# Kernel optimization log

Measured on AMD Instinct MI355X. Metric: run time of the kernel, lower is better.

The kernel has to match this reference:

```python
import jax, jax.numpy as jnp
import numpy as np

B, T_ENC, T_DEC = 16, 256, 64
N_MEL = 80
ENC_DIM = 512
ATTN_RNN_DIM = 1024
DEC_RNN_DIM = 1024
PRENET_DIM = 256
ATTN_DIM = 128
LOC_FILTERS = 32
LOC_KERNEL = 31


def setup_inputs() -> dict:
    key = jax.random.key(0)
    ks = jax.random.split(key, 32)
    s = 0.02
    inp = {
        "memory": jax.random.normal(ks[0], (B, T_ENC, ENC_DIM), jnp.float32),
        "decoder_inputs": jax.random.normal(ks[1], (B, N_MEL, T_DEC), jnp.float32),
        "memory_lengths": jax.random.randint(ks[2], (B,), T_ENC // 2, T_ENC + 1, jnp.int32),
        # prenet
        "prenet_W1": jax.random.normal(ks[3], (PRENET_DIM, N_MEL), jnp.float32) * s,
        "prenet_b1": jnp.zeros((PRENET_DIM,), jnp.float32),
        "prenet_W2": jax.random.normal(ks[4], (PRENET_DIM, PRENET_DIM), jnp.float32) * s,
        "prenet_b2": jnp.zeros((PRENET_DIM,), jnp.float32),
        # attention LSTMCell: input = prenet_dim + enc_dim
        "attn_rnn_Wih": jax.random.normal(ks[5], (4 * ATTN_RNN_DIM, PRENET_DIM + ENC_DIM), jnp.float32) * s,
        "attn_rnn_Whh": jax.random.normal(ks[6], (4 * ATTN_RNN_DIM, ATTN_RNN_DIM), jnp.float32) * s,
        "attn_rnn_bih": jnp.zeros((4 * ATTN_RNN_DIM,), jnp.float32),
        "attn_rnn_bhh": jnp.zeros((4 * ATTN_RNN_DIM,), jnp.float32),
        # attention projections (bias-free, Tacotron2 style)
        "query_W": jax.random.normal(ks[7], (ATTN_DIM, ATTN_RNN_DIM), jnp.float32) * s,
        "mem_W": jax.random.normal(ks[8], (ATTN_DIM, ENC_DIM), jnp.float32) * s,
        "loc_conv_W": jax.random.normal(ks[9], (LOC_FILTERS, 2, LOC_KERNEL), jnp.float32) * s,
        "loc_dense_W": jax.random.normal(ks[10], (ATTN_DIM, LOC_FILTERS), jnp.float32) * s,
        "attn_v": jax.random.normal(ks[11], (1, ATTN_DIM), jnp.float32) * s,
        # decoder LSTMCell: input = attn_rnn_dim + enc_dim
        "dec_rnn_Wih": jax.random.normal(ks[12], (4 * DEC_RNN_DIM, ATTN_RNN_DIM + ENC_DIM), jnp.float32) * s,
        "dec_rnn_Whh": jax.random.normal(ks[13], (4 * DEC_RNN_DIM, DEC_RNN_DIM), jnp.float32) * s,
        "dec_rnn_bih": jnp.zeros((4 * DEC_RNN_DIM,), jnp.float32),
        "dec_rnn_bhh": jnp.zeros((4 * DEC_RNN_DIM,), jnp.float32),
        # output heads
        "proj_W": jax.random.normal(ks[14], (N_MEL, DEC_RNN_DIM + ENC_DIM), jnp.float32) * s,
        "proj_b": jnp.zeros((N_MEL,), jnp.float32),
        "gate_W": jax.random.normal(ks[15], (1, DEC_RNN_DIM + ENC_DIM), jnp.float32) * s,
        "gate_b": jnp.zeros((1,), jnp.float32),
    }
    return inp


def _lstm_cell(x, h, c, Wih, Whh, bih, bhh):
    gates = x @ Wih.T + bih + h @ Whh.T + bhh  # [B, 4H]
    i, f, g, o = jnp.split(gates, 4, axis=-1)
    c2 = jax.nn.sigmoid(f) * c + jax.nn.sigmoid(i) * jnp.tanh(g)
    h2 = jax.nn.sigmoid(o) * jnp.tanh(c2)
    return h2, c2


def _decoder_forward(memory, decoder_inputs, memory_lengths,
                     prenet_W1, prenet_b1, prenet_W2, prenet_b2,
                     attn_rnn_Wih, attn_rnn_Whh, attn_rnn_bih, attn_rnn_bhh,
                     query_W, mem_W, loc_conv_W, loc_dense_W, attn_v,
                     dec_rnn_Wih, dec_rnn_Whh, dec_rnn_bih, dec_rnn_bhh,
                     proj_W, proj_b, gate_W, gate_b):
    b, t_enc, _ = memory.shape
    t_dec = decoder_inputs.shape[2]
    # parse_decoder_inputs: [B,80,T] -> [T,B,80]; prepend go frame
    frames = jnp.transpose(decoder_inputs, (2, 0, 1))  # [T,B,80]
    go = jnp.zeros((1, b, N_MEL), frames.dtype)
    frames = jnp.concatenate([go, frames], axis=0)  # [T+1,B,80]
    # prenet (dropout disabled for determinism)
    pre = jax.nn.relu(frames @ prenet_W1.T + prenet_b1)
    pre = jax.nn.relu(pre @ prenet_W2.T + prenet_b2)  # [T+1,B,256]
    pre = pre[:-1]  # steps use frames 0..T-1

    processed_memory = memory @ mem_W.T  # [B,T_enc,128]
    pad_mask = jnp.arange(t_enc)[None, :] >= memory_lengths[:, None]  # [B,T_enc] True=pad

    pad = (LOC_KERNEL - 1) // 2

    def step(carry, x_t):
        (ah, ac, dh, dc, aw, aw_cum, ctx) = carry
        cell_in = jnp.concatenate([x_t, ctx], axis=-1)
        ah, ac = _lstm_cell(cell_in, ah, ac, attn_rnn_Wih, attn_rnn_Whh, attn_rnn_bih, attn_rnn_bhh)
        # location-sensitive attention
        awc = jnp.stack([aw, aw_cum], axis=1)  # [B,2,T_enc]
        loc = jax.lax.conv_general_dilated(
            awc, loc_conv_W, window_strides=(1,), padding=[(pad, pad)],
            dimension_numbers=("NCH", "OIH", "NCH"))  # [B,32,T_enc]
        loc = jnp.transpose(loc, (0, 2, 1)) @ loc_dense_W.T  # [B,T_enc,128]
        query = (ah @ query_W.T)[:, None, :]  # [B,1,128]
        energies = jnp.squeeze(jnp.tanh(query + processed_memory + loc) @ attn_v.T, -1)  # [B,T_enc]
        energies = jnp.where(pad_mask, -1e9, energies)
        aw = jax.nn.softmax(energies, axis=1)
        ctx = jnp.einsum("bt,btd->bd", aw, memory)
        aw_cum = aw_cum + aw
        dec_in = jnp.concatenate([ah, ctx], axis=-1)
        dh, dc = _lstm_cell(dec_in, dh, dc, dec_rnn_Wih, dec_rnn_Whh, dec_rnn_bih, dec_rnn_bhh)
        dhc = jnp.concatenate([dh, ctx], axis=-1)
        mel = dhc @ proj_W.T + proj_b  # [B,80]
        gate = jnp.squeeze(dhc @ gate_W.T + gate_b, -1)  # [B]
        return (ah, ac, dh, dc, aw, aw_cum, ctx), (mel, gate, aw)

    z = jnp.zeros
    carry0 = (z((b, ATTN_RNN_DIM)), z((b, ATTN_RNN_DIM)),
              z((b, DEC_RNN_DIM)), z((b, DEC_RNN_DIM)),
              z((b, t_enc)), z((b, t_enc)), z((b, ENC_DIM)))
    _, (mels, gates, aligns) = jax.lax.scan(step, carry0, pre)
    # parse_decoder_outputs
    mel_outputs = jnp.transpose(mels, (1, 2, 0))  # [B,80,T_dec]
    gate_outputs = jnp.transpose(gates, (1, 0))  # [B,T_dec]
    alignments = jnp.transpose(aligns, (1, 0, 2))  # [B,T_dec,T_enc]
    return mel_outputs, gate_outputs, alignments


def reference(memory, decoder_inputs, memory_lengths,
              prenet_W1, prenet_b1, prenet_W2, prenet_b2,
              attn_rnn_Wih, attn_rnn_Whh, attn_rnn_bih, attn_rnn_bhh,
              query_W, mem_W, loc_conv_W, loc_dense_W, attn_v,
              dec_rnn_Wih, dec_rnn_Whh, dec_rnn_bih, dec_rnn_bhh,
              proj_W, proj_b, gate_W, gate_b):
    return _decoder_forward(memory, decoder_inputs, memory_lengths,
                            prenet_W1, prenet_b1, prenet_W2, prenet_b2,
                            attn_rnn_Wih, attn_rnn_Whh, attn_rnn_bih, attn_rnn_bhh,
                            query_W, mem_W, loc_conv_W, loc_dense_W, attn_v,
                            dec_rnn_Wih, dec_rnn_Whh, dec_rnn_bih, dec_rnn_bhh,
                            proj_W, proj_b, gate_W, gate_b)
```

## Files before the change

### kernel.cpp

```cpp
#include <hip/hip_runtime.h>

typedef __attribute__((ext_vector_type(8))) short short8;
typedef __attribute__((ext_vector_type(4))) float f32x4;
typedef unsigned short u16;
typedef unsigned int u32;
typedef unsigned long long u64;


static constexpr size_t OFF_WFA   = 0;
static constexpr size_t OFF_WFD   = 14680064;
static constexpr size_t OFF_PREF  = 35651584;
static constexpr size_t OFF_QWB   = 36175872;
static constexpr size_t OFF_MWT   = 36438016;
static constexpr size_t OFF_BA    = 36700160;
static constexpr size_t OFF_BD    = 36716544;
static constexpr size_t OFF_PM    = 36732928;
static constexpr size_t OFF_CTXF  = 38830080;
static constexpr size_t OFF_DHF   = 40960000;
static constexpr size_t OFF_AHFD  = 45219840;
static constexpr size_t OFF_CTXFD = 47349760;
static constexpr size_t OFF_DHFD  = 48414720;
static constexpr size_t OFF_BAR   = 50544640;
static constexpr size_t OFF_END   = 50548736;

__device__ __forceinline__ float sigmf(float x) { return 1.f / (1.f + expf(-x)); }
__device__ __forceinline__ float tanh_fast(float x) {
  float e2 = __expf(2.f * x);
  return 1.f - 2.f / (e2 + 1.f);
}
__device__ __forceinline__ u16 f2bf(float f) {
  u32 u = __float_as_uint(f);
  return (u16)((u + 0x7FFFu + ((u >> 16) & 1u)) >> 16);
}
__device__ __forceinline__ float bf2f(u16 x) { return __uint_as_float(((u32)x) << 16); }

__device__ __forceinline__ short8 ld_frag_nt(const void* p) {
  const u64* q = (const u64*)p;
  u64 lo = __builtin_nontemporal_load(q);
  u64 hi = __builtin_nontemporal_load(q + 1);
  union { u64 q2[2]; short8 s; } u;
  u.q2[0] = lo; u.q2[1] = hi;
  return u.s;
}

__device__ __forceinline__ void st_u16_agent(u16* p, u16 v) {
  __hip_atomic_store(p, v, __ATOMIC_RELAXED, __HIP_MEMORY_SCOPE_AGENT);
}
__device__ __forceinline__ void st_f32_agent(float* p, float v) {
  __hip_atomic_store(p, v, __ATOMIC_RELAXED, __HIP_MEMORY_SCOPE_AGENT);
}
__device__ __forceinline__ u32 ld_u32_agent(const u32* p) {
  return __hip_atomic_load(p, __ATOMIC_RELAXED, __HIP_MEMORY_SCOPE_AGENT);
}
__device__ __forceinline__ void st_u32_agent(u32* p, u32 v) {
  __hip_atomic_store(p, v, __ATOMIC_RELAXED, __HIP_MEMORY_SCOPE_AGENT);
}

template <int SLP>
__device__ __forceinline__ void wait_p128(const u32* F, u32 target, int th) {
  if (th < 64) {
    for (;;) {
      u32 v0 = ld_u32_agent(F + th);
      u32 v1 = ld_u32_agent(F + 64 + th);
      u32 mn = v0 < v1 ? v0 : v1;
      if (__all(mn >= target)) break;
      __builtin_amdgcn_s_sleep(SLP);
    }
  }
  __syncthreads();
}
template <int SLP>
__device__ __forceinline__ void wait_s16(const u32* F, u32 target, int th) {
  if (th < 64) {
    const u32* pf = F + (th & 15) * 16;
    for (;;) {
      u32 v = ld_u32_agent(pf);
      if (__all(v >= target)) break;
      __builtin_amdgcn_s_sleep(SLP);
    }
  }
  __syncthreads();
}

__global__ void k_wfrag(const float* __restrict__ Wih, const float* __restrict__ Whh,
                        char* __restrict__ dst, int NT, int Kih) {
  int idx = blockIdx.x * 256 + threadIdx.x;
  int l = idx & 63;
  int st = idx >> 6;
  int s = st % NT, tile = st / NT;
  int r = l & 15, kg = l >> 4;
  int j = (r >> 2) * 1024 + tile * 4 + (r & 3);
  int k0 = s * 32 + kg * 8;
  const float* src = (k0 < Kih) ? (Wih + (size_t)j * Kih + k0)
                                : (Whh + (size_t)j * 1024 + (k0 - Kih));
  short8 v;
#pragma unroll
  for (int e = 0; e < 8; ++e) v[e] = (short)f2bf(src[e]);
  *(short8*)(dst + (size_t)idx * 16) = v;
}

__global__ void k_smallprep(const float* __restrict__ memW,
                            const float* __restrict__ abih, const float* __restrict__ abhh,
                            const float* __restrict__ dbih, const float* __restrict__ dbhh,
                            const float* __restrict__ qW, char* __restrict__ wsb) {
  int idx = blockIdx.x * 256 + threadIdx.x;
  if (idx < 65536) {
    int k = idx >> 7, d = idx & 127;
    ((float*)(wsb + OFF_MWT))[idx] = memW[d * 512 + k];
  } else if (idx < 69632) {
    int j = idx - 65536;
    ((float*)(wsb + OFF_BA))[j] = abih[j] + abhh[j];
  } else if (idx < 73728) {
    int j = idx - 69632;
    ((float*)(wsb + OFF_BD))[j] = dbih[j] + dbhh[j];
  } else if (idx < 204800) {
    int j = idx - 73728;
    ((u16*)(wsb + OFF_QWB))[j] = f2bf(qW[j]);
  }
}

__global__ void k_prenet(const float* __restrict__ dec_in,
                         const float* __restrict__ W1, const float* __restrict__ b1,
                         const float* __restrict__ W2, const float* __restrict__ b2,
                         char* __restrict__ wsb) {
  int s = blockIdx.x, b = blockIdx.y, th = threadIdx.x;
  __shared__ float frame[80];
  __shared__ float h1[256];
  if (th < 80) frame[th] = (s == 0) ? 0.f : dec_in[(b * 80 + th) * 64 + (s - 1)];
  __syncthreads();
  float a = b1[th];
  const float* w1r = W1 + th * 80;
  for (int m = 0; m < 80; ++m) a += w1r[m] * frame[m];
  h1[th] = fmaxf(a, 0.f);
  __syncthreads();
  float a2 = b2[th];
  const float* w2r = W2 + th * 256;
  for (int i = 0; i < 256; ++i) a2 += w2r[i] * h1[i];
  float pre = fmaxf(a2, 0.f);
  int k = th;
  ((u16*)(wsb + OFF_PREF))[(((size_t)s * 8 + (k >> 5)) * 64 + ((k >> 3) & 3) * 16 + b) * 8 + (k & 7)] = f2bf(pre);
}

__global__ void k_pm(const float* __restrict__ memory, char* __restrict__ wsb) {
  int bk = blockIdx.x, th = threadIdx.x;
  int b = bk >> 4, t0 = (bk & 15) * 16;
  __shared__ float mrow[16 * 512];
  for (int i = 0; i < 8; ++i) {
    int fi4 = i * 256 + th;
    int tl = fi4 >> 7, k4 = (fi4 & 127) << 2;
    *(float4*)&mrow[tl * 512 + k4] =
        *(const float4*)&memory[((size_t)(b * 256 + t0 + tl)) * 512 + k4];
  }
  __syncthreads();
  int d = th & 127, tl0 = th >> 7;
  float acc[8] = {};
  const float* mWT = (const float*)(wsb + OFF_MWT);
  float* pmw = (float*)(wsb + OFF_PM);
  for (int k = 0; k < 512; ++k) {
    float w = mWT[k * 128 + d];
#pragma unroll
    for (int i = 0; i < 8; ++i) acc[i] += w * mrow[(tl0 + i * 2) * 512 + k];
  }
  for (int i = 0; i < 8; ++i)
    pmw[((size_t)(b * 256 + t0 + tl0 + i * 2)) * 128 + d] = acc[i];
}

struct KParams {
  const float* memory;
  const int* mlen;
  const float* convW;
  const float* ldW;
  const float* attnv;
  const float* projW;
  const float* projb;
  const float* gateW;
  const float* gateb;
  char* wsb;
  float* out;
};

__device__ __forceinline__ f32x4 attn_early(char* wsb, int t, int kc, int l,
                                            const short8* afE) {
  f32x4 acc = {0.f, 0.f, 0.f, 0.f};
#pragma unroll
  for (int i = 0; i < 10; ++i) {
    int pe = kc * 10 + i;
    const char* src = (pe < 8)
        ? wsb + OFF_PREF + (((size_t)t * 8 + pe) * 64 + l) * 16
        : wsb + OFF_AHFD + (((size_t)t * 32 + (pe - 8)) * 64 + l) * 16;
    short8 bv = ld_frag_nt(src);
    acc = __builtin_amdgcn_mfma_f32_16x16x32_bf16(afE[i], bv, acc, 0, 0, 0);
  }
  return acc;
}

__device__ __forceinline__ void run_dec(char* wsb, int t, int tb, int th, int l, int w,
                                        int rt, int kc, float biasD_r, float& cD,
                                        float* smC) {
  const char* wfd = wsb + OFF_WFD;
  int tIdx = tb * 2 + rt;
  f32x4 acc = {0.f, 0.f, 0.f, 0.f};
#pragma unroll
  for (int i = 0; i < 20; ++i) {
    int kt = kc * 20 + i;
    short8 av = *(const short8*)(wfd + (((size_t)tIdx * 80 + kt) * 64 + l) * 16);
    const char* src;
    if (kt < 32)      src = wsb + OFF_AHFD + (((size_t)t * 32 + kt) * 64 + l) * 16;
    else if (kt < 48) src = wsb + OFF_CTXFD + (((size_t)t * 16 + (kt - 32)) * 64 + l) * 16;
    else              src = wsb + OFF_DHFD + (((size_t)(t - 1) * 32 + (kt - 48)) * 64 + l) * 16;
    short8 bv = ld_frag_nt(src);
    acc = __builtin_amdgcn_mfma_f32_16x16x32_bf16(av, bv, acc, 0, 0, 0);
  }
#pragma unroll
  for (int r4 = 0; r4 < 4; ++r4)
    smC[w * 256 + ((l >> 4) * 4 + r4) * 16 + (l & 15)] = acc[r4];
  __syncthreads();
  {
    int rt2 = th >> 8, r = (th >> 4) & 15, b2 = th & 15;
    float s = 0.f;
#pragma unroll
    for (int q = 0; q < 4; ++q) s += smC[(q * 2 + rt2) * 256 + r * 16 + b2];
    smC[4096 + th] = s + biasD_r;
  }
  __syncthreads();
  if (th < 128) {
    int b = th & 15, lu = th >> 4;
    int rt3 = lu >> 2, ul = lu & 3;
    int u = (tb * 2 + rt3) * 4 + ul;
    float gi = smC[4096 + rt3 * 256 + ul * 16 + b];
    float gf = smC[4096 + rt3 * 256 + (4 + ul) * 16 + b];
    float gc = smC[4096 + rt3 * 256 + (8 + ul) * 16 + b];
    float go = smC[4096 + rt3 * 256 + (12 + ul) * 16 + b];
    float c2 = sigmf(gf) * cD + sigmf(gi) * tanhf(gc);
    float h2 = sigmf(go) * tanhf(c2);
    cD = c2;
    st_f32_agent((float*)(wsb + OFF_DHF) + ((size_t)t * 1024 + u) * 16 + b, h2);
    st_u16_agent((u16*)(wsb + OFF_DHFD) +
                 ((((size_t)t * 32 + (u >> 5)) * 64 + ((u >> 3) & 3) * 16 + b) * 8 + (u & 7)),
                 f2bf(h2));
  }
}

__global__ void __launch_bounds__(512, 1) k_main(KParams p) {
  const int th = threadIdx.x;
  const int bk = blockIdx.x;
  char* wsb = p.wsb;
  const int l = th & 63, w = th >> 6;
  u32* Af = (u32*)(wsb + OFF_BAR);
  u32* Df = (u32*)(wsb + OFF_BAR + 1024);
  u32* Bf = (u32*)(wsb + OFF_BAR + 2048);

  __shared__ float smC[4608];
  __shared__ float s2q[128], s2v[128];
  __shared__ u16 s_convF[8192];
  __shared__ __align__(16) float s2ah[1024];
  __shared__ float s_e[256], s3wr[4];
  __shared__ float s1cw[1984];
  __shared__ float s_aw[256], s_awc[256];

  const float* pm = (const float*)(wsb + OFF_PM);
  const u16* qwb = (const u16*)(wsb + OFF_QWB);

  if (bk < 16) {
    for (int i = th; i < 1984; i += 512) s1cw[i] = p.convW[i];
    for (int i = th; i < 4096; i += 512) ((u32*)s_convF)[i] = 0u;
    if (th < 128) s2v[th] = p.attnv[th];
    if (th < 256) { s_aw[th] = 0.f; s_awc[th] = 0.f; }
  }

  float biasA_r = 0.f, biasD_r = 0.f;
  if (bk >= 16 && bk < 144) {
    int r = (th >> 4) & 15, rt2 = th >> 8, tbase = (bk - 16) * 2;
    biasA_r = ((const float*)(wsb + OFF_BA))[(r >> 2) * 1024 + (tbase + rt2) * 4 + (r & 3)];
    biasD_r = ((const float*)(wsb + OFF_BD))[(r >> 2) * 1024 + (tbase + rt2) * 4 + (r & 3)];
  }
  int lenB = 0;
  if (bk < 16) lenB = p.mlen[bk];
  float cA = 0.f, cD = 0.f;

  const int rt = w & 1, kc = w >> 1;
  short8 afE[10], afL[4];
  if (bk >= 16 && bk < 144) {
    const char* wfa = wsb + OFF_WFA;
    int tIdx = (bk - 16) * 2 + rt;
#pragma unroll
    for (int i = 0; i < 10; ++i) {
      int pe = kc * 10 + i;
      int kt = (pe < 8) ? pe : (24 + (pe - 8));
      afE[i] = *(const short8*)(wfa + (((size_t)tIdx * 56 + kt) * 64 + l) * 16);
    }
#pragma unroll
    for (int i = 0; i < 4; ++i) {
      int kt = 8 + kc * 4 + i;
      afL[i] = *(const short8*)(wfa + (((size_t)tIdx * 56 + kt) * 64 + l) * 16);
    }
  }
  short8 ldwB[8];
  if (bk < 16) {
    int kg = l >> 4, dcol = l & 15;
#pragma unroll
    for (int dt = 0; dt < 8; ++dt) {
      short8 v;
#pragma unroll
      for (int e = 0; e < 8; ++e)
        v[e] = (short)f2bf(p.ldW[(dt * 16 + dcol) * 32 + kg * 8 + e]);
      ldwB[dt] = v;
    }
  }
  __syncthreads();

  if (bk >= 16 && bk < 144) {
    const int tb = bk - 16;
    f32x4 acc = attn_early(wsb, 0, kc, l, afE);
    for (int t = 0; t < 64; ++t) {
      wait_s16<4>(Bf, (u32)t, th);
#pragma unroll
      for (int i = 0; i < 4; ++i) {
        int ct = kc * 4 + i;
        short8 bv = ld_frag_nt(wsb + OFF_CTXFD + (((size_t)t * 16 + ct) * 64 + l) * 16);
        acc = __builtin_amdgcn_mfma_f32_16x16x32_bf16(afL[i], bv, acc, 0, 0, 0);
      }
#pragma unroll
      for (int r4 = 0; r4 < 4; ++r4)
        smC[w * 256 + ((l >> 4) * 4 + r4) * 16 + (l & 15)] = acc[r4];
      __syncthreads();
      {
        int rt2 = th >> 8, r = (th >> 4) & 15, b2 = th & 15;
        float s = 0.f;
#pragma unroll
        for (int q = 0; q < 4; ++q) s += smC[(q * 2 + rt2) * 256 + r * 16 + b2];
        smC[4096 + th] = s + biasA_r;
      }
      __syncthreads();
      if (th < 128) {
        int b = th & 15, lu = th >> 4;
        int rt3 = lu >> 2, ul = lu & 3;
        int u = (tb * 2 + rt3) * 4 + ul;
        float gi = smC[4096 + rt3 * 256 + ul * 16 + b];
        float gf = smC[4096 + rt3 * 256 + (4 + ul) * 16 + b];
        float gc = smC[4096 + rt3 * 256 + (8 + ul) * 16 + b];
        float go = smC[4096 + rt3 * 256 + (12 + ul) * 16 + b];
        float c2 = sigmf(gf) * cA + sigmf(gi) * tanhf(gc);
        float h2 = sigmf(go) * tanhf(c2);
        cA = c2;
        st_u16_agent((u16*)(wsb + OFF_AHFD) +
                     ((((size_t)(t + 1) * 32 + (u >> 5)) * 64 + ((u >> 3) & 3) * 16 + b) * 8 + (u & 7)),
                     f2bf(h2));
      }
      __syncthreads();
      if (th == 0) st_u32_agent(Af + tb, (u32)(t + 1));
      if (t >= 1) {
        wait_p128<4>(Df, (u32)(t - 1), th);
        run_dec(wsb, t, tb, th, l, w, rt, kc, biasD_r, cD, smC);
        __syncthreads();
        if (th == 0) st_u32_agent(Df + tb, (u32)t);
      }
      if (t < 63) {
        wait_p128<4>(Af, (u32)(t + 1), th);
        acc = attn_early(wsb, t + 1, kc, l, afE);
      }
    }
    wait_s16<4>(Bf, 64u, th);
    wait_p128<4>(Df, 63u, th);
    run_dec(wsb, 64, tb, th, l, w, rt, kc, biasD_r, cD, smC);
    __syncthreads();
    if (th == 0) st_u32_agent(Df + tb, 64u);
  } else if (bk < 16) {
    const int b = bk;
    for (int t = 0; t < 64; ++t) {
      {
        int jmax = (lenB + 15) >> 4;
        for (int j = 0; j < jmax; ++j) {
          int idx = j * 512 + th, tt = idx >> 5, f = idx & 31;
          float a = 0.f;
          const float* w0 = s1cw + f * 62;
#pragma unroll
          for (int kk = 0; kk < 31; ++kk) {
            int pos = tt + kk - 15;
            bool ok = (pos >= 0 && pos < 256);
            float awv = ok ? s_aw[pos] : 0.f;
            float awcv = ok ? s_awc[pos] : 0.f;
            a += awv * w0[kk] + awcv * w0[31 + kk];
          }
          s_convF[(tt >> 4) * 512 + ((f >> 3) * 16 + (tt & 15)) * 8 + (f & 7)] = f2bf(a);
        }
      }
      wait_p128<4>(Af, (u32)(t + 1), th);
      if (th < 128) {
        int o = th;
        short8 v = ld_frag_nt(wsb + OFF_AHFD +
                    (((size_t)(t + 1) * 32 + (o >> 2)) * 64 + (o & 3) * 16 + b) * 16);
#pragma unroll
        for (int e = 0; e < 8; ++e) s2ah[o * 8 + e] = bf2f((u16)v[e]);
      }
      __syncthreads();
      {
        int d = th & 127, part = th >> 7;
        const u16* qr = qwb + d * 1024 + part * 256;
        const float* ah = s2ah + part * 256;
        float qa = 0.f;
        for (int kk = 0; kk < 256; kk += 8) {
          short8 v = *(const short8*)(qr + kk);
#pragma unroll
          for (int e = 0; e < 8; ++e) qa += bf2f((u16)v[e]) * ah[kk + e];
        }
        smC[part * 128 + d] = qa;
      }
      __syncthreads();
      if (th < 128) s2q[th] = smC[th] + smC[128 + th] + smC[256 + th] + smC[384 + th];
      __syncthreads();
      {
#pragma unroll
        for (int tl = 0; tl < 2; ++tl) {
          int ttile = w * 2 + tl;
          short8 afc = *(const short8*)&s_convF[ttile * 512 + l * 8];
          int dcol = l & 15;
          float e0 = 0.f, e1 = 0.f, e2 = 0.f, e3 = 0.f;
          const float* pmb = pm + ((size_t)(b * 256 + ttile * 16 + (l >> 4) * 4)) * 128 + dcol;
#pragma unroll
          for (int dt = 0; dt < 8; ++dt) {
            f32x4 S = {0.f, 0.f, 0.f, 0.f};
            S = __builtin_amdgcn_mfma_f32_16x16x32_bf16(afc, ldwB[dt], S, 0, 0, 0);
            int d = dt * 16 + dcol;
            float qd = s2q[d], vd = s2v[d];
            e0 += vd * tanh_fast(qd + pmb[dt * 16 + 0 * 128] + S[0]);
            e1 += vd * tanh_fast(qd + pmb[dt * 16 + 1 * 128] + S[1]);
            e2 += vd * tanh_fast(qd + pmb[dt * 16 + 2 * 128] + S[2]);
            e3 += vd * tanh_fast(qd + pmb[dt * 16 + 3 * 128] + S[3]);
          }
#pragma unroll
          for (int off = 8; off; off >>= 1) {
            e0 += __shfl_xor(e0, off);
            e1 += __shfl_xor(e1, off);
            e2 += __shfl_xor(e2, off);
            e3 += __shfl_xor(e3, off);
          }
          if ((l & 15) == 0) {
            int tb0 = ttile * 16 + (l >> 4) * 4;
            s_e[tb0]     = (tb0     < lenB) ? __expf(e0) : 0.f;
            s_e[tb0 + 1] = (tb0 + 1 < lenB) ? __expf(e1) : 0.f;
            s_e[tb0 + 2] = (tb0 + 2 < lenB) ? __expf(e2) : 0.f;
            s_e[tb0 + 3] = (tb0 + 3 < lenB) ? __expf(e3) : 0.f;
          }
        }
      }
      __syncthreads();
      if (th < 256) {
        float v0 = s_e[th];
#pragma unroll
        for (int off = 32; off; off >>= 1) v0 += __shfl_xor(v0, off);
        if ((th & 63) == 0) s3wr[th >> 6] = v0;
      }
      __syncthreads();
      float rden = 1.f / (s3wr[0] + s3wr[1] + s3wr[2] + s3wr[3]);
      if (th < 256) {
        float a = s_e[th] * rden;
        s_aw[th] = a;
        s_awc[th] += a;
        p.out[82944 + ((size_t)(b * 64 + t)) * 256 + th] = a;
      }
      __syncthreads();
      {
        int dq = th & 127, tg = th >> 7;
        int d0 = dq * 4;
        float a0 = 0.f, a1 = 0.f, a2 = 0.f, a3 = 0.f;
        const float* mb = p.memory + ((size_t)b * 256) * 512 + d0;
        for (int tt = tg; tt < lenB; tt += 4) {
          float4 mv = *(const float4*)(mb + (size_t)tt * 512);
          float aw = s_aw[tt];
          a0 += aw * mv.x; a1 += aw * mv.y; a2 += aw * mv.z; a3 += aw * mv.w;
        }
        smC[tg * 512 + d0]     = a0;
        smC[tg * 512 + d0 + 1] = a1;
        smC[tg * 512 + d0 + 2] = a2;
        smC[tg * 512 + d0 + 3] = a3;
      }
      __syncthreads();
      {
        int d = th;
        float ctxv = smC[d] + smC[512 + d] + smC[1024 + d] + smC[1536 + d];
        st_f32_agent((float*)(wsb + OFF_CTXF) + ((size_t)(t + 1) * 512 + d) * 16 + b, ctxv);
        st_u16_agent((u16*)(wsb + OFF_CTXFD) +
                     ((((size_t)(t + 1) * 16 + (d >> 5)) * 64 + ((d >> 3) & 3) * 16 + b) * 8 + (d & 7)),
                     f2bf(ctxv));
      }
      __syncthreads();
      if (th == 0) st_u32_agent(Bf + b * 16, (u32)(t + 1));
    }
  }

  if (bk >= 144) {
    wait_p128<96>(Df, 64u, th);
    wait_s16<96>(Bf, 64u, th);
  } else {
    wait_p128<8>(Df, 64u, th);
    wait_s16<8>(Bf, 64u, th);
  }
  {
    int t = bk & 63, pa = bk >> 6;
    const float* dh = (const float*)(wsb + OFF_DHF) + (size_t)(t + 1) * 16384;
    const float* cx = (const float*)(wsb + OFF_CTXF) + (size_t)(t + 1) * 8192;
    int lim = (pa == 3) ? 336 : 320;
    for (int idx = th; idx < lim; idx += 512) {
      if (idx < 320) {
        int mi = idx >> 4, b = idx & 15, m = pa * 20 + mi;
        const float* wr = p.projW + (size_t)m * 1536;
        float a0 = 0.f, a1 = 0.f;
#pragma unroll 8
        for (int k = 0; k < 1024; k += 2) { a0 += wr[k] * dh[k * 16 + b]; a1 += wr[k + 1] * dh[(k + 1) * 16 + b]; }
#pragma unroll 8
        for (int k = 0; k < 512; k += 2)  { a0 += wr[1024 + k] * cx[k * 16 + b]; a1 += wr[1025 + k] * cx[(k + 1) * 16 + b]; }
        p.out[((size_t)(b * 80 + m)) * 64 + t] = a0 + a1 + p.projb[m];
      } else {
        int b = idx - 320;
        float a0 = 0.f, a1 = 0.f;
#pragma unroll 8
        for (int k = 0; k < 1024; k += 2) { a0 += p.gateW[k] * dh[k * 16 + b]; a1 += p.gateW[k + 1] * dh[(k + 1) * 16 + b]; }
#pragma unroll 8
        for (int k = 0; k < 512; k += 2)  { a0 += p.gateW[1024 + k] * cx[k * 16 + b]; a1 += p.gateW[1025 + k] * cx[(k + 1) * 16 + b]; }
        p.out[81920 + b * 64 + t] = a0 + a1 + p.gateb[0];
      }
    }
  }
}

extern "C" void kernel_launch(void* const* d_in, const int* in_sizes, int n_in,
                              void* d_out, int out_size, void* d_ws, size_t ws_size,
                              hipStream_t stream) {
  (void)in_sizes; (void)n_in; (void)out_size; (void)ws_size;
  const float* memory = (const float*)d_in[0];
  const float* dec_in = (const float*)d_in[1];
  const int*   mlen   = (const int*)d_in[2];
  const float* pW1    = (const float*)d_in[3];
  const float* pb1    = (const float*)d_in[4];
  const float* pW2    = (const float*)d_in[5];
  const float* pb2    = (const float*)d_in[6];
  const float* aWih   = (const float*)d_in[7];
  const float* aWhh   = (const float*)d_in[8];
  const float* abih   = (const float*)d_in[9];
  const float* abhh   = (const float*)d_in[10];
  const float* qW     = (const float*)d_in[11];
  const float* memW   = (const float*)d_in[12];
  const float* convW  = (const float*)d_in[13];
  const float* ldW    = (const float*)d_in[14];
  const float* attnv  = (const float*)d_in[15];
  const float* dWih   = (const float*)d_in[16];
  const float* dWhh   = (const float*)d_in[17];
  const float* dbih   = (const float*)d_in[18];
  const float* dbhh   = (const float*)d_in[19];
  const float* projW  = (const float*)d_in[20];
  const float* projb  = (const float*)d_in[21];
  const float* gateW  = (const float*)d_in[22];
  const float* gateb  = (const float*)d_in[23];
  char* wsb = (char*)d_ws;
  float* out = (float*)d_out;

  hipMemsetAsync(wsb + OFF_AHFD, 0, 32768, stream);
  hipMemsetAsync(wsb + OFF_CTXFD, 0, 16384, stream);
  hipMemsetAsync(wsb + OFF_DHFD, 0, 32768, stream);
  hipMemsetAsync(wsb + OFF_BAR, 0, 4096, stream);

  hipLaunchKernelGGL(k_wfrag, dim3(3584), dim3(256), 0, stream, aWih, aWhh, wsb + OFF_WFA, 56, 768);
  hipLaunchKernelGGL(k_wfrag, dim3(5120), dim3(256), 0, stream, dWih, dWhh, wsb + OFF_WFD, 80, 1536);
  hipLaunchKernelGGL(k_smallprep, dim3(800), dim3(256), 0, stream, memW, abih, abhh, dbih, dbhh, qW, wsb);
  hipLaunchKernelGGL(k_prenet, dim3(64, 16), dim3(256), 0, stream, dec_in, pW1, pb1, pW2, pb2, wsb);
  hipLaunchKernelGGL(k_pm, dim3(256), dim3(256), 0, stream, memory, wsb);

  KParams p{memory, mlen, convW, ldW, attnv, projW, projb, gateW, gateb, wsb, out};
  void* args[] = { &p };
  hipLaunchCooperativeKernel((void*)k_main, dim3(256), dim3(512), args, 0, stream);
}
```

Measured before the change: 2.826 ms.

## Aggregate barrier flags via dedicated blocks, MFMA query projection, packed fragment stores

Three idle blocks (144-146) now poll the per-block attention, decoder and context progress flags and publish one aggregate counter each. Worker blocks spin on that single word instead of having a whole wavefront scan 128 flags. The query projection is moved from a scalar bf16 dot product to MFMA over pre-laid-out query-weight fragments. Hidden and context bf16 fragments are staged in shared memory and written as 64-bit stores rather than scattered 16-bit ones, and the fp32 context layout is changed to make the projection reads contiguous. The cost is an extra hop of latency through the aggregator blocks and more __syncthreads per step.

```diff
diff --git a/kernel.cpp b/kernel.cpp
--- a/kernel.cpp
+++ b/kernel.cpp
@@ -10,7 +10,7 @@
 static constexpr size_t OFF_WFA   = 0;
 static constexpr size_t OFF_WFD   = 14680064;
 static constexpr size_t OFF_PREF  = 35651584;
-static constexpr size_t OFF_QWB   = 36175872;
+static constexpr size_t OFF_QWF   = 36175872;
 static constexpr size_t OFF_MWT   = 36438016;
 static constexpr size_t OFF_BA    = 36700160;
 static constexpr size_t OFF_BD    = 36716544;
@@ -49,6 +49,9 @@
 __device__ __forceinline__ void st_f32_agent(float* p, float v) {
   __hip_atomic_store(p, v, __ATOMIC_RELAXED, __HIP_MEMORY_SCOPE_AGENT);
 }
+__device__ __forceinline__ void st_u64_agent(u64* p, u64 v) {
+  __hip_atomic_store(p, v, __ATOMIC_RELAXED, __HIP_MEMORY_SCOPE_AGENT);
+}
 __device__ __forceinline__ u32 ld_u32_agent(const u32* p) {
   return __hip_atomic_load(p, __ATOMIC_RELAXED, __HIP_MEMORY_SCOPE_AGENT);
 }
@@ -57,27 +60,9 @@
 }
 
 template <int SLP>
-__device__ __forceinline__ void wait_p128(const u32* F, u32 target, int th) {
-  if (th < 64) {
-    for (;;) {
-      u32 v0 = ld_u32_agent(F + th);
-      u32 v1 = ld_u32_agent(F + 64 + th);
-      u32 mn = v0 < v1 ? v0 : v1;
-      if (__all(mn >= target)) break;
-      __builtin_amdgcn_s_sleep(SLP);
-    }
-  }
-  __syncthreads();
-}
-template <int SLP>
-__device__ __forceinline__ void wait_s16(const u32* F, u32 target, int th) {
-  if (th < 64) {
-    const u32* pf = F + (th & 15) * 16;
-    for (;;) {
-      u32 v = ld_u32_agent(pf);
-      if (__all(v >= target)) break;
-      __builtin_amdgcn_s_sleep(SLP);
-    }
+__device__ __forceinline__ void wait_one(const u32* f, u32 target, int th) {
+  if (th == 0) {
+    while (ld_u32_agent(f) < target) __builtin_amdgcn_s_sleep(SLP);
   }
   __syncthreads();
 }
@@ -99,10 +84,22 @@
   *(short8*)(dst + (size_t)idx * 16) = v;
 }
 
+__global__ void k_qwfrag(const float* __restrict__ qW, char* __restrict__ dst) {
+  int idx = blockIdx.x * 256 + threadIdx.x;
+  int l = idx & 63, tile = idx >> 6;
+  int dt = tile >> 5, kt = tile & 31;
+  int j = dt * 16 + (l & 15);
+  int k0 = kt * 32 + (l >> 4) * 8;
+  short8 v;
+#pragma unroll
+  for (int e = 0; e < 8; ++e) v[e] = (short)f2bf(qW[j * 1024 + k0 + e]);
+  *(short8*)(dst + (size_t)idx * 16) = v;
+}
+
 __global__ void k_smallprep(const float* __restrict__ memW,
                             const float* __restrict__ abih, const float* __restrict__ abhh,
                             const float* __restrict__ dbih, const float* __restrict__ dbhh,
-                            const float* __restrict__ qW, char* __restrict__ wsb) {
+                            char* __restrict__ wsb) {
   int idx = blockIdx.x * 256 + threadIdx.x;
   if (idx < 65536) {
     int k = idx >> 7, d = idx & 127;
@@ -113,9 +110,6 @@
   } else if (idx < 73728) {
     int j = idx - 69632;
     ((float*)(wsb + OFF_BD))[j] = dbih[j] + dbhh[j];
-  } else if (idx < 204800) {
-    int j = idx - 73728;
-    ((u16*)(wsb + OFF_QWB))[j] = f2bf(qW[j]);
   }
 }
 
@@ -249,17 +243,19 @@
   u32* Af = (u32*)(wsb + OFF_BAR);
   u32* Df = (u32*)(wsb + OFF_BAR + 1024);
   u32* Bf = (u32*)(wsb + OFF_BAR + 2048);
+  u32* Aall = (u32*)(wsb + OFF_BAR + 3072);
+  u32* Dall = (u32*)(wsb + OFF_BAR + 3136);
+  u32* Ball = (u32*)(wsb + OFF_BAR + 3200);
 
   __shared__ float smC[4608];
   __shared__ float s2q[128], s2v[128];
   __shared__ u16 s_convF[8192];
-  __shared__ __align__(16) float s2ah[1024];
+  __shared__ u16 s_pack[512];
   __shared__ float s_e[256], s3wr[4];
   __shared__ float s1cw[1984];
   __shared__ float s_aw[256], s_awc[256];
 
   const float* pm = (const float*)(wsb + OFF_PM);
-  const u16* qwb = (const u16*)(wsb + OFF_QWB);
 
   if (bk < 16) {
     for (int i = th; i < 1984; i += 512) s1cw[i] = p.convW[i];
@@ -313,7 +309,7 @@
     const int tb = bk - 16;
     f32x4 acc = attn_early(wsb, 0, kc, l, afE);
     for (int t = 0; t < 64; ++t) {
-      wait_s16<4>(Bf, (u32)t, th);
+      wait_one<1>(Ball, (u32)t, th);
 #pragma unroll
       for (int i = 0; i < 4; ++i) {
         int ct = kc * 4 + i;
@@ -334,34 +330,38 @@
       __syncthreads();
       if (th < 128) {
         int b = th & 15, lu = th >> 4;
-        int rt3 = lu >> 2, ul = lu & 3;
-        int u = (tb * 2 + rt3) * 4 + ul;
-        float gi = smC[4096 + rt3 * 256 + ul * 16 + b];
-        float gf = smC[4096 + rt3 * 256 + (4 + ul) * 16 + b];
-        float gc = smC[4096 + rt3 * 256 + (8 + ul) * 16 + b];
-        float go = smC[4096 + rt3 * 256 + (12 + ul) * 16 + b];
+        float gi = smC[4096 + (lu >> 2) * 256 + (lu & 3) * 16 + b];
+        float gf = smC[4096 + (lu >> 2) * 256 + (4 + (lu & 3)) * 16 + b];
+        float gc = smC[4096 + (lu >> 2) * 256 + (8 + (lu & 3)) * 16 + b];
+        float go = smC[4096 + (lu >> 2) * 256 + (12 + (lu & 3)) * 16 + b];
         float c2 = sigmf(gf) * cA + sigmf(gi) * tanhf(gc);
         float h2 = sigmf(go) * tanhf(c2);
         cA = c2;
-        st_u16_agent((u16*)(wsb + OFF_AHFD) +
-                     ((((size_t)(t + 1) * 32 + (u >> 5)) * 64 + ((u >> 3) & 3) * 16 + b) * 8 + (u & 7)),
-                     f2bf(h2));
+        s_pack[b * 8 + lu] = f2bf(h2);
+      }
+      __syncthreads();
+      if (th < 16) {
+        const u64* src = (const u64*)s_pack + th * 2;
+        u64* dst = (u64*)(wsb + OFF_AHFD + ((size_t)(t + 1) * 32 + (tb >> 2)) * 1024 +
+                          ((size_t)(tb & 3) * 16 + th) * 16);
+        st_u64_agent(dst, src[0]);
+        st_u64_agent(dst + 1, src[1]);
       }
       __syncthreads();
       if (th == 0) st_u32_agent(Af + tb, (u32)(t + 1));
       if (t >= 1) {
-        wait_p128<4>(Df, (u32)(t - 1), th);
+        wait_one<1>(Dall, (u32)(t - 1), th);
         run_dec(wsb, t, tb, th, l, w, rt, kc, biasD_r, cD, smC);
         __syncthreads();
         if (th == 0) st_u32_agent(Df + tb, (u32)t);
       }
       if (t < 63) {
-        wait_p128<4>(Af, (u32)(t + 1), th);
+        wait_one<1>(Aall, (u32)(t + 1), th);
         acc = attn_early(wsb, t + 1, kc, l, afE);
       }
     }
-    wait_s16<4>(Bf, 64u, th);
-    wait_p128<4>(Df, 63u, th);
+    wait_one<1>(Ball, 64u, th);
+    wait_one<1>(Dall, 63u, th);
     run_dec(wsb, 64, tb, th, l, w, rt, kc, biasD_r, cD, smC);
     __syncthreads();
     if (th == 0) st_u32_agent(Df + tb, 64u);
@@ -385,29 +385,25 @@
           s_convF[(tt >> 4) * 512 + ((f >> 3) * 16 + (tt & 15)) * 8 + (f & 7)] = f2bf(a);
         }
       }
-      wait_p128<4>(Af, (u32)(t + 1), th);
-      if (th < 128) {
-        int o = th;
-        short8 v = ld_frag_nt(wsb + OFF_AHFD +
-                    (((size_t)(t + 1) * 32 + (o >> 2)) * 64 + (o & 3) * 16 + b) * 16);
-#pragma unroll
-        for (int e = 0; e < 8; ++e) s2ah[o * 8 + e] = bf2f((u16)v[e]);
-      }
-      __syncthreads();
+      wait_one<1>(Aall, (u32)(t + 1), th);
       {
-        int d = th & 127, part = th >> 7;
-        const u16* qr = qwb + d * 1024 + part * 256;
-        const float* ah = s2ah + part * 256;
-        float qa = 0.f;
-        for (int kk = 0; kk < 256; kk += 8) {
-          short8 v = *(const short8*)(qr + kk);
-#pragma unroll
-          for (int e = 0; e < 8; ++e) qa += bf2f((u16)v[e]) * ah[kk + e];
-        }
-        smC[part * 128 + d] = qa;
-      }
-      __syncthreads();
-      if (th < 128) s2q[th] = smC[th] + smC[128 + th] + smC[256 + th] + smC[384 + th];
+        f32x4 qacc = {0.f, 0.f, 0.f, 0.f};
+        const char* qwf = wsb + OFF_QWF;
+#pragma unroll 4
+        for (int kt = 0; kt < 32; ++kt) {
+          short8 av = *(const short8*)(qwf + (((size_t)w * 32 + kt) * 64 + l) * 16);
+          short8 bv = ld_frag_nt(wsb + OFF_AHFD + ((size_t)(t + 1) * 32 + kt) * 1024 +
+                                 ((size_t)(l >> 4) * 16 + b) * 16);
+          qacc = __builtin_amdgcn_mfma_f32_16x16x32_bf16(av, bv, qacc, 0, 0, 0);
+        }
+        if ((l & 15) == 0) {
+          int r0 = (l >> 4) * 4;
+          s2q[w * 16 + r0]     = qacc[0];
+          s2q[w * 16 + r0 + 1] = qacc[1];
+          s2q[w * 16 + r0 + 2] = qacc[2];
+          s2q[w * 16 + r0 + 3] = qacc[3];
+        }
+      }
       __syncthreads();
       {
 #pragma unroll
@@ -479,45 +475,94 @@
       {
         int d = th;
         float ctxv = smC[d] + smC[512 + d] + smC[1024 + d] + smC[1536 + d];
-        st_f32_agent((float*)(wsb + OFF_CTXF) + ((size_t)(t + 1) * 512 + d) * 16 + b, ctxv);
-        st_u16_agent((u16*)(wsb + OFF_CTXFD) +
-                     ((((size_t)(t + 1) * 16 + (d >> 5)) * 64 + ((d >> 3) & 3) * 16 + b) * 8 + (d & 7)),
-                     f2bf(ctxv));
+        st_f32_agent((float*)(wsb + OFF_CTXF) + (size_t)(t + 1) * 8192 + b * 512 + d, ctxv);
+        s_pack[d] = f2bf(ctxv);
+      }
+      __syncthreads();
+      if (th < 64) {
+        u64 p0 = ((const u64*)s_pack)[th * 2];
+        u64 p1 = ((const u64*)s_pack)[th * 2 + 1];
+        u64* dst = (u64*)(wsb + OFF_CTXFD + ((size_t)(t + 1) * 16 + (th >> 2)) * 1024 +
+                          ((size_t)(th & 3) * 16 + b) * 16);
+        st_u64_agent(dst, p0);
+        st_u64_agent(dst + 1, p1);
       }
       __syncthreads();
       if (th == 0) st_u32_agent(Bf + b * 16, (u32)(t + 1));
     }
-  }
-
-  if (bk >= 144) {
-    wait_p128<96>(Df, 64u, th);
-    wait_s16<96>(Bf, 64u, th);
+  } else if (bk == 144) {
+    if (th < 64) {
+      for (u32 tgt = 1; tgt <= 64; ++tgt) {
+        for (;;) {
+          u32 v0 = ld_u32_agent(Af + th);
+          u32 v1 = ld_u32_agent(Af + 64 + th);
+          u32 mn = v0 < v1 ? v0 : v1;
+          if (__all(mn >= tgt)) break;
+          __builtin_amdgcn_s_sleep(1);
+        }
+        if (th == 0) st_u32_agent(Aall, tgt);
+      }
+    }
+    __syncthreads();
+  } else if (bk == 145) {
+    if (th < 64) {
+      for (u32 tgt = 1; tgt <= 64; ++tgt) {
+        for (;;) {
+          u32 v0 = ld_u32_agent(Df + th);
+          u32 v1 = ld_u32_agent(Df + 64 + th);
+          u32 mn = v0 < v1 ? v0 : v1;
+          if (__all(mn >= tgt)) break;
+          __builtin_amdgcn_s_sleep(1);
+        }
+        if (th == 0) st_u32_agent(Dall, tgt);
+      }
+    }
+    __syncthreads();
+  } else if (bk == 146) {
+    if (th < 64) {
+      for (u32 tgt = 1; tgt <= 64; ++tgt) {
+        for (;;) {
+          u32 v = ld_u32_agent(Bf + (th & 15) * 16);
+          if (__all(v >= tgt)) break;
+          __builtin_amdgcn_s_sleep(1);
+        }
+        if (th == 0) st_u32_agent(Ball, tgt);
+      }
+    }
+    __syncthreads();
+  }
+
+  if (bk >= 147) {
+    wait_one<64>(Dall, 64u, th);
+    wait_one<64>(Ball, 64u, th);
   } else {
-    wait_p128<8>(Df, 64u, th);
-    wait_s16<8>(Bf, 64u, th);
+    wait_one<4>(Dall, 64u, th);
+    wait_one<4>(Ball, 64u, th);
   }
   {
     int t = bk & 63, pa = bk >> 6;
     const float* dh = (const float*)(wsb + OFF_DHF) + (size_t)(t + 1) * 16384;
-    const float* cx = (const float*)(wsb + OFF_CTXF) + (size_t)(t + 1) * 8192;
+    const float* cxt = (const float*)(wsb + OFF_CTXF) + (size_t)(t + 1) * 8192;
     int lim = (pa == 3) ? 336 : 320;
     for (int idx = th; idx < lim; idx += 512) {
       if (idx < 320) {
         int mi = idx >> 4, b = idx & 15, m = pa * 20 + mi;
         const float* wr = p.projW + (size_t)m * 1536;
+        const float* cxb = cxt + b * 512;
         float a0 = 0.f, a1 = 0.f;
 #pragma unroll 8
         for (int k = 0; k < 1024; k += 2) { a0 += wr[k] * dh[k * 16 + b]; a1 += wr[k + 1] * dh[(k + 1) * 16 + b]; }
 #pragma unroll 8
-        for (int k = 0; k < 512; k += 2)  { a0 += wr[1024 + k] * cx[k * 16 + b]; a1 += wr[1025 + k] * cx[(k + 1) * 16 + b]; }
+        for (int k = 0; k < 512; k += 2)  { a0 += wr[1024 + k] * cxb[k]; a1 += wr[1025 + k] * cxb[k + 1]; }
         p.out[((size_t)(b * 80 + m)) * 64 + t] = a0 + a1 + p.projb[m];
       } else {
         int b = idx - 320;
+        const float* cxb = cxt + b * 512;
         float a0 = 0.f, a1 = 0.f;
 #pragma unroll 8
         for (int k = 0; k < 1024; k += 2) { a0 += p.gateW[k] * dh[k * 16 + b]; a1 += p.gateW[k + 1] * dh[(k + 1) * 16 + b]; }
 #pragma unroll 8
-        for (int k = 0; k < 512; k += 2)  { a0 += p.gateW[1024 + k] * cx[k * 16 + b]; a1 += p.gateW[1025 + k] * cx[(k + 1) * 16 + b]; }
+        for (int k = 0; k < 512; k += 2)  { a0 += p.gateW[1024 + k] * cxb[k]; a1 += p.gateW[1025 + k] * cxb[k + 1]; }
         p.out[81920 + b * 64 + t] = a0 + a1 + p.gateb[0];
       }
     }
@@ -562,7 +607,8 @@
 
   hipLaunchKernelGGL(k_wfrag, dim3(3584), dim3(256), 0, stream, aWih, aWhh, wsb + OFF_WFA, 56, 768);
   hipLaunchKernelGGL(k_wfrag, dim3(5120), dim3(256), 0, stream, dWih, dWhh, wsb + OFF_WFD, 80, 1536);
-  hipLaunchKernelGGL(k_smallprep, dim3(800), dim3(256), 0, stream, memW, abih, abhh, dbih, dbhh, qW, wsb);
+  hipLaunchKernelGGL(k_qwfrag, dim3(64), dim3(256), 0, stream, qW, wsb + OFF_QWF);
+  hipLaunchKernelGGL(k_smallprep, dim3(288), dim3(256), 0, stream, memW, abih, abhh, dbih, dbhh, wsb);
   hipLaunchKernelGGL(k_prenet, dim3(64, 16), dim3(256), 0, stream, dec_in, pW1, pb1, pW2, pb2, wsb);
   hipLaunchKernelGGL(k_pm, dim3(256), dim3(256), 0, stream, memory, wsb);
 
```

Result: no change. 2.783 ms (-1.5%).
